# Performance work log

Measured on AMD Instinct MI355X. Metric: run time of the kernel, lower is better.

The kernel has to match this reference:

```python
import jax, jax.numpy as jnp
import numpy as np

N = 100000   # nodes
E = 1600000  # edges
F = 128      # input node features
H = 128      # hidden channels
G = 512      # graphs in batch
EPS = 1e-5   # BatchNorm eps


def setup_inputs() -> dict:
    key = jax.random.key(0)
    ks = jax.random.split(key, 24)
    x = jax.random.normal(ks[0], (N, F), jnp.float32)
    edge_index = jax.random.randint(ks[1], (2, E), 0, N)
    batch = jnp.sort(jax.random.randint(ks[2], (N,), 0, G))

    def lin_w(k, i, o):
        return jax.random.normal(k, (i, o), jnp.float32) / np.sqrt(i)

    inp = {
        "x": x, "edge_index": edge_index, "batch": batch,
        "W1": lin_w(ks[3], F, H), "b1": jnp.zeros((H,), jnp.float32),
        "g1": jnp.ones((H,), jnp.float32), "be1": jnp.zeros((H,), jnp.float32),
        "m1": 0.1 * jax.random.normal(ks[4], (H,), jnp.float32),
        "v1": jax.random.uniform(ks[5], (H,), jnp.float32) + 0.5,
        "W2": lin_w(ks[6], H, H), "b2": jnp.zeros((H,), jnp.float32),
        "g2": jnp.ones((H,), jnp.float32), "be2": jnp.zeros((H,), jnp.float32),
        "m2": 0.1 * jax.random.normal(ks[7], (H,), jnp.float32),
        "v2": jax.random.uniform(ks[8], (H,), jnp.float32) + 0.5,
        "W3": lin_w(ks[9], H, H), "b3": jnp.zeros((H,), jnp.float32),
        "g3": jnp.ones((H,), jnp.float32), "be3": jnp.zeros((H,), jnp.float32),
        "m3": 0.1 * jax.random.normal(ks[10], (H,), jnp.float32),
        "v3": jax.random.uniform(ks[11], (H,), jnp.float32) + 0.5,
        "Wl": lin_w(ks[12], H, 1), "bl": jnp.zeros((1,), jnp.float32),
    }
    return inp


def _gcn_norm(edge_index):
    # add self-loops, then symmetric normalization deg^-1/2 A_hat deg^-1/2
    loops = jnp.arange(N)
    src = jnp.concatenate([edge_index[0], loops])
    dst = jnp.concatenate([edge_index[1], loops])
    deg = jax.ops.segment_sum(jnp.ones_like(src, jnp.float32), dst, num_segments=N)
    dinv = jax.lax.rsqrt(jnp.maximum(deg, 1.0))
    norm = dinv[src] * dinv[dst]  # [E+N]
    return src, dst, norm


def _gcn_conv(x, W, b, src, dst, norm):
    h = x @ W                                    # [N,H] dense GEMM first (PyG order)
    msg = h[src] * norm[:, None]                 # gather + scale, [E+N,H]
    agg = jax.ops.segment_sum(msg, dst, num_segments=N)  # scatter-add
    return agg + b


def _bn_relu(x, g, be, m, v):
    # inference BatchNorm1d (running stats) + ReLU
    return jax.nn.relu((x - m) * jax.lax.rsqrt(v + EPS) * g + be)


def reference(x, edge_index, batch,
              W1, b1, g1, be1, m1, v1,
              W2, b2, g2, be2, m2, v2,
              W3, b3, g3, be3, m3, v3,
              Wl, bl):
    src, dst, norm = _gcn_norm(edge_index)
    h = _bn_relu(_gcn_conv(x, W1, b1, src, dst, norm), g1, be1, m1, v1)
    h = _bn_relu(_gcn_conv(h, W2, b2, src, dst, norm), g2, be2, m2, v2)
    h = _bn_relu(_gcn_conv(h, W3, b3, src, dst, norm), g3, be3, m3, v3)
    # global mean pool over graphs
    sums = jax.ops.segment_sum(h, batch, num_segments=G)           # [G,H]
    cnt = jax.ops.segment_sum(jnp.ones((N,), jnp.float32), batch, num_segments=G)
    pooled = sums / jnp.maximum(cnt, 1.0)[:, None]
    # dropout is identity at inference; final linear
    return pooled @ Wl + bl  # [G,1]
```

## Files before the change

### kernel.cpp

```cpp
#include <hip/hip_runtime.h>
#include <hip/hip_bf16.h>

#define NN 100000
#define NE 1600000
#define HD 128
#define NG 512
#define BN_EPS 1e-5f

typedef __attribute__((ext_vector_type(8))) short short8;
typedef __attribute__((ext_vector_type(4))) float floatx4;

__device__ __forceinline__ ushort f2bf(float f) {
    union { float f; uint u; } v; v.f = f;
    uint r = (v.u + 0x7FFF + ((v.u >> 16) & 1)) >> 16;
    return (ushort)r;
}
__device__ __forceinline__ float bflo(uint u) { union { uint u; float f; } v; v.u = u << 16; return v.f; }
__device__ __forceinline__ float bfhi(uint u) { union { uint u; float f; } v; v.u = u & 0xFFFF0000u; return v.f; }

__global__ void k_zero_i(int* p, int n) {
    int i = blockIdx.x * 256 + threadIdx.x;
    if (i < n) p[i] = 0;
}

__global__ void k_hist_rank(const int* __restrict__ dst, int* __restrict__ indeg,
                            int* __restrict__ rank) {
    int e = blockIdx.x * 256 + threadIdx.x;
    if (e < NE) rank[e] = atomicAdd(&indeg[dst[e]], 1);
}

__global__ void k_dinv(const int* __restrict__ indeg, float* __restrict__ dinv) {
    int i = blockIdx.x * 256 + threadIdx.x;
    if (i < NN) dinv[i] = rsqrtf((float)(indeg[i] + 1));
}

__global__ void k_scan1(const int* __restrict__ indeg, int* __restrict__ rs, int* __restrict__ aux) {
    __shared__ int s[256];
    int t = threadIdx.x;
    int base = blockIdx.x * 1024 + t * 4;
    int v0 = 0, v1 = 0, v2 = 0, v3 = 0;
    if (base + 0 < NN) v0 = indeg[base + 0];
    if (base + 1 < NN) v1 = indeg[base + 1];
    if (base + 2 < NN) v2 = indeg[base + 2];
    if (base + 3 < NN) v3 = indeg[base + 3];
    int tsum = v0 + v1 + v2 + v3;
    s[t] = tsum;
    __syncthreads();
    for (int o = 1; o < 256; o <<= 1) {
        int x = 0;
        if (t >= o) x = s[t - o];
        __syncthreads();
        s[t] += x;
        __syncthreads();
    }
    int excl = s[t] - tsum;
    if (base + 0 < NN) rs[base + 0] = excl;
    if (base + 1 < NN) rs[base + 1] = excl + v0;
    if (base + 2 < NN) rs[base + 2] = excl + v0 + v1;
    if (base + 3 < NN) rs[base + 3] = excl + v0 + v1 + v2;
    if (t == 255) aux[blockIdx.x] = s[255];
}

__global__ void k_scan2(int* __restrict__ aux, int nblk) {
    __shared__ int s[128];
    int t = threadIdx.x;
    int v = (t < nblk) ? aux[t] : 0;
    s[t] = v;
    __syncthreads();
    for (int o = 1; o < 128; o <<= 1) {
        int x = 0;
        if (t >= o) x = s[t - o];
        __syncthreads();
        s[t] += x;
        __syncthreads();
    }
    if (t < nblk) aux[t] = s[t] - v;
}

__global__ void k_scan3(int* __restrict__ rs, const int* __restrict__ aux) {
    int i = blockIdx.x * 256 + threadIdx.x;
    if (i < NN) rs[i] += aux[i >> 10];
    if (i == 0) rs[NN] = NE;
}

__global__ void k_fill(const int* __restrict__ src, const int* __restrict__ dst,
                       const int* __restrict__ rank, const int* __restrict__ rs,
                       int* __restrict__ csr) {
    int e = blockIdx.x * 256 + threadIdx.x;
    if (e >= NE) return;
    csr[rs[dst[e]] + rank[e]] = src[e];
}

__global__ void k_bn_prep(const float* __restrict__ b, const float* __restrict__ g,
                          const float* __restrict__ be, const float* __restrict__ m,
                          const float* __restrict__ v, float* scale, float* shift) {
    int f = threadIdx.x;
    if (f < HD) {
        float sc = g[f] * rsqrtf(v[f] + BN_EPS);
        scale[f] = sc;
        shift[f] = (b[f] - m[f]) * sc + be[f];
    }
}

__global__ void k_gstart(const int* __restrict__ batch, int* __restrict__ gstart) {
    int g = blockIdx.x * 256 + threadIdx.x;
    if (g > NG) return;
    if (g == NG) { gstart[NG] = NN; return; }
    int lo = 0, hi = NN;
    while (lo < hi) {
        int mid = (lo + hi) >> 1;
        if (batch[mid] < g) lo = mid + 1; else hi = mid;
    }
    gstart[g] = lo;
}

__global__ void k_cast(const float* __restrict__ x, ushort* __restrict__ xb) {
    long i = (long)(blockIdx.x * 256 + threadIdx.x) * 4;
    if (i >= (long)NN * 128) return;
    float4 v = *(const float4*)(x + i);
    uint2 o;
    o.x = (uint)f2bf(v.x) | ((uint)f2bf(v.y) << 16);
    o.y = (uint)f2bf(v.z) | ((uint)f2bf(v.w) << 16);
    *(uint2*)(xb + i) = o;
}

#define WT_STRIDE 136
__launch_bounds__(256)
__global__ void k_gemm_mfma(const ushort* __restrict__ xb, const float* __restrict__ W,
                            const float* __restrict__ dinv, ushort* __restrict__ hs) {
    __shared__ ushort sWt[128 * WT_STRIDE];
    const int tid = threadIdx.x;
    for (int i = tid; i < 128 * 128; i += 256) {
        int k = i >> 7, n = i & 127;
        sWt[n * WT_STRIDE + k] = f2bf(W[i]);
    }
    __syncthreads();

    const int wave = tid >> 6, lane = tid & 63;
    const int m = lane & 15, kg = lane >> 4;
    const long row0 = (long)blockIdx.x * 64 + wave * 16;

    long arow = row0 + m;
    long arc = arow < NN ? arow : (NN - 1);
    short8 a[4];
#pragma unroll
    for (int s = 0; s < 4; ++s)
        a[s] = *(const short8*)(xb + arc * 128 + s * 32 + kg * 8);

    floatx4 acc[8];
#pragma unroll
    for (int ct = 0; ct < 8; ++ct) acc[ct] = (floatx4){0.f, 0.f, 0.f, 0.f};

#pragma unroll
    for (int s = 0; s < 4; ++s) {
#pragma unroll
        for (int ct = 0; ct < 8; ++ct) {
            short8 b = *(const short8*)&sWt[(ct * 16 + m) * WT_STRIDE + s * 32 + kg * 8];
            acc[ct] = __builtin_amdgcn_mfma_f32_16x16x32_bf16(a[s], b, acc[ct], 0, 0, 0);
        }
    }

#pragma unroll
    for (int r = 0; r < 4; ++r) {
        long orow = row0 + kg * 4 + r;
        if (orow < NN) {
            float dd = dinv[orow];
#pragma unroll
            for (int ct = 0; ct < 8; ++ct)
                hs[orow * 128 + ct * 16 + m] = f2bf(acc[ct][r] * dd);
        }
    }
}

__global__ void k_gather_bf(const ushort* __restrict__ hs, const int* __restrict__ rs,
                            const int* __restrict__ csr, const float* __restrict__ dinv,
                            const float* __restrict__ scale, const float* __restrict__ shift,
                            ushort* __restrict__ xout) {
    int t = blockIdx.x * 256 + threadIdx.x;
    int d = t >> 4;
    if (d >= NN) return;
    int lane = t & 15;
    int c0 = lane * 8;
    int e0 = rs[d], e1 = rs[d + 1];

    uint4 sv = *(const uint4*)(hs + (long)d * 128 + c0);
    float a0 = bflo(sv.x), a1 = bfhi(sv.x), a2 = bflo(sv.y), a3 = bfhi(sv.y);
    float a4 = bflo(sv.z), a5 = bfhi(sv.z), a6 = bflo(sv.w), a7 = bfhi(sv.w);

    int j = e0;
    for (; j + 1 < e1; j += 2) {
        int s0 = csr[j], s1 = csr[j + 1];
        uint4 v0 = *(const uint4*)(hs + (long)s0 * 128 + c0);
        uint4 v1 = *(const uint4*)(hs + (long)s1 * 128 + c0);
        a0 += bflo(v0.x) + bflo(v1.x); a1 += bfhi(v0.x) + bfhi(v1.x);
        a2 += bflo(v0.y) + bflo(v1.y); a3 += bfhi(v0.y) + bfhi(v1.y);
        a4 += bflo(v0.z) + bflo(v1.z); a5 += bfhi(v0.z) + bfhi(v1.z);
        a6 += bflo(v0.w) + bflo(v1.w); a7 += bfhi(v0.w) + bfhi(v1.w);
    }
    if (j < e1) {
        int s0 = csr[j];
        uint4 v0 = *(const uint4*)(hs + (long)s0 * 128 + c0);
        a0 += bflo(v0.x); a1 += bfhi(v0.x);
        a2 += bflo(v0.y); a3 += bfhi(v0.y);
        a4 += bflo(v0.z); a5 += bfhi(v0.z);
        a6 += bflo(v0.w); a7 += bfhi(v0.w);
    }

    float dd = dinv[d];
    float4 sca = *(const float4*)(scale + c0);
    float4 scb = *(const float4*)(scale + c0 + 4);
    float4 sha = *(const float4*)(shift + c0);
    float4 shb = *(const float4*)(shift + c0 + 4);
    float r0 = fmaxf(dd * a0 * sca.x + sha.x, 0.f);
    float r1 = fmaxf(dd * a1 * sca.y + sha.y, 0.f);
    float r2 = fmaxf(dd * a2 * sca.z + sha.z, 0.f);
    float r3 = fmaxf(dd * a3 * sca.w + sha.w, 0.f);
    float r4 = fmaxf(dd * a4 * scb.x + shb.x, 0.f);
    float r5 = fmaxf(dd * a5 * scb.y + shb.y, 0.f);
    float r6 = fmaxf(dd * a6 * scb.z + shb.z, 0.f);
    float r7 = fmaxf(dd * a7 * scb.w + shb.w, 0.f);
    uint4 o;
    o.x = (uint)f2bf(r0) | ((uint)f2bf(r1) << 16);
    o.y = (uint)f2bf(r2) | ((uint)f2bf(r3) << 16);
    o.z = (uint)f2bf(r4) | ((uint)f2bf(r5) << 16);
    o.w = (uint)f2bf(r6) | ((uint)f2bf(r7) << 16);
    *(uint4*)(xout + (long)d * 128 + c0) = o;
}

__global__ void k_pool_final2(const ushort* __restrict__ x, const int* __restrict__ gstart,
                              const float* __restrict__ Wl, const float* __restrict__ bl,
                              float* __restrict__ out) {
    __shared__ float red[256];
    int g = blockIdx.x;
    int tid = threadIdx.x;
    int f = tid & 127;
    int half = tid >> 7;
    int i0 = gstart[g], i1 = gstart[g + 1];

    float acc = 0.f;
    for (int i = i0 + half; i < i1; i += 2) {
        union { uint u; float f; } v; v.u = (uint)x[(long)i * 128 + f] << 16;
        acc += v.f;
    }
    red[tid] = acc;
    __syncthreads();
    if (tid < 128) red[tid] = (red[tid] + red[tid + 128]) * Wl[tid];
    __syncthreads();
    for (int o = 64; o > 0; o >>= 1) {
        if (tid < o) red[tid] += red[tid + o];
        __syncthreads();
    }
    if (tid == 0) out[g] = red[0] / fmaxf((float)(i1 - i0), 1.f) + bl[0];
}

extern "C" void kernel_launch(void* const* d_in, const int* in_sizes, int n_in,
                              void* d_out, int out_size, void* d_ws, size_t ws_size,
                              hipStream_t stream) {
    const float* x   = (const float*)d_in[0];
    const int*   ei  = (const int*)d_in[1];
    const int*   bat = (const int*)d_in[2];
    const float* W1  = (const float*)d_in[3];
    const float* b1  = (const float*)d_in[4];
    const float* g1  = (const float*)d_in[5];
    const float* be1 = (const float*)d_in[6];
    const float* m1  = (const float*)d_in[7];
    const float* v1  = (const float*)d_in[8];
    const float* W2  = (const float*)d_in[9];
    const float* b2  = (const float*)d_in[10];
    const float* g2  = (const float*)d_in[11];
    const float* be2 = (const float*)d_in[12];
    const float* m2  = (const float*)d_in[13];
    const float* v2  = (const float*)d_in[14];
    const float* W3  = (const float*)d_in[15];
    const float* b3  = (const float*)d_in[16];
    const float* g3  = (const float*)d_in[17];
    const float* be3 = (const float*)d_in[18];
    const float* m3  = (const float*)d_in[19];
    const float* v3  = (const float*)d_in[20];
    const float* Wl  = (const float*)d_in[21];
    const float* bl  = (const float*)d_in[22];
    float* out = (float*)d_out;

    const int* srcp = ei;
    const int* dstp = ei + NE;

    char* ws = (char*)d_ws;
    size_t off = 0;
    auto alloc = [&](size_t bytes) { char* p = ws + off; off += (bytes + 255) & ~255ULL; return p; };
    float*  dinv   = (float*) alloc(NN * 4);
    int*    indeg  = (int*)   alloc(NN * 4);
    int*    rs     = (int*)   alloc((NN + 1) * 4);
    int*    aux    = (int*)   alloc(128 * 4);
    int*    csr    = (int*)   alloc(NE * 4);
    int*    rank   = (int*)   alloc(NE * 4);
    float*  scale1 = (float*) alloc(HD * 4);
    float*  shift1 = (float*) alloc(HD * 4);
    float*  scale2 = (float*) alloc(HD * 4);
    float*  shift2 = (float*) alloc(HD * 4);
    float*  scale3 = (float*) alloc(HD * 4);
    float*  shift3 = (float*) alloc(HD * 4);
    int*    gstart = (int*)   alloc((NG + 1) * 4);
    ushort* xb     = (ushort*)alloc((size_t)NN * HD * 2);
    ushort* hs     = (ushort*)alloc((size_t)NN * HD * 2);
    ushort* xbuf   = (ushort*)alloc((size_t)NN * HD * 2);

    const int nblk_scan = (NN + 1023) / 1024;
    const int grid_n    = (NN + 255) / 256;
    const int grid_e    = (NE + 255) / 256;
    const int gemm_grid = (NN + 63) / 64;
    const int gath_grid = (NN * 16 + 255) / 256;
    const int cast_grid = (NN * 128 / 4 + 255) / 256;

    k_zero_i<<<grid_n, 256, 0, stream>>>(indeg, NN);
    k_hist_rank<<<grid_e, 256, 0, stream>>>(dstp, indeg, rank);
    k_dinv<<<grid_n, 256, 0, stream>>>(indeg, dinv);
    k_scan1<<<nblk_scan, 256, 0, stream>>>(indeg, rs, aux);
    k_scan2<<<1, 128, 0, stream>>>(aux, nblk_scan);
    k_scan3<<<grid_n, 256, 0, stream>>>(rs, aux);
    k_fill<<<grid_e, 256, 0, stream>>>(srcp, dstp, rank, rs, csr);

    k_bn_prep<<<1, 128, 0, stream>>>(b1, g1, be1, m1, v1, scale1, shift1);
    k_bn_prep<<<1, 128, 0, stream>>>(b2, g2, be2, m2, v2, scale2, shift2);
    k_bn_prep<<<1, 128, 0, stream>>>(b3, g3, be3, m3, v3, scale3, shift3);
    k_gstart<<<3, 256, 0, stream>>>(bat, gstart);
    k_cast<<<cast_grid, 256, 0, stream>>>(x, xb);

    k_gemm_mfma<<<gemm_grid, 256, 0, stream>>>(xb, W1, dinv, hs);
    k_gather_bf<<<gath_grid, 256, 0, stream>>>(hs, rs, csr, dinv, scale1, shift1, xbuf);
    k_gemm_mfma<<<gemm_grid, 256, 0, stream>>>(xbuf, W2, dinv, hs);
    k_gather_bf<<<gath_grid, 256, 0, stream>>>(hs, rs, csr, dinv, scale2, shift2, xbuf);
    k_gemm_mfma<<<gemm_grid, 256, 0, stream>>>(xbuf, W3, dinv, hs);
    k_gather_bf<<<gath_grid, 256, 0, stream>>>(hs, rs, csr, dinv, scale3, shift3, xbuf);

    k_pool_final2<<<NG, 256, 0, stream>>>(xbuf, gstart, Wl, bl, out);
}
```

Before: 524.8 us.

## Fuse input cast into GEMM, pretranspose weights, stage epilogue, unroll gather

Removes the separate fp32-to-bf16 cast pass by converting x inside the first GEMM's A-load. Weights are transposed and converted once per layer into global buffers instead of being rebuilt in shared memory by every GEMM block, so B fragments now come from global/L2. The GEMM epilogue is staged through shared memory so rows are written with coalesced 16-byte stores. The gather loop is unrolled to four neighbours for more memory-level parallelism. Reading B from global instead of LDS may add L2 traffic.

```diff
diff --git a/kernel.cpp b/kernel.cpp
--- a/kernel.cpp
+++ b/kernel.cpp
@@ -114,38 +114,47 @@
     gstart[g] = lo;
 }
 
-__global__ void k_cast(const float* __restrict__ x, ushort* __restrict__ xb) {
-    long i = (long)(blockIdx.x * 256 + threadIdx.x) * 4;
-    if (i >= (long)NN * 128) return;
-    float4 v = *(const float4*)(x + i);
-    uint2 o;
-    o.x = (uint)f2bf(v.x) | ((uint)f2bf(v.y) << 16);
-    o.y = (uint)f2bf(v.z) | ((uint)f2bf(v.w) << 16);
-    *(uint2*)(xb + i) = o;
-}
-
-#define WT_STRIDE 136
+__global__ void k_prep_w(const float* __restrict__ W, ushort* __restrict__ Wt) {
+    int i = blockIdx.x * 256 + threadIdx.x;
+    if (i < 128 * 128) {
+        int k = i >> 7, n = i & 127;
+        Wt[n * 128 + k] = f2bf(W[i]);
+    }
+}
+
+template <bool F32>
 __launch_bounds__(256)
-__global__ void k_gemm_mfma(const ushort* __restrict__ xb, const float* __restrict__ W,
-                            const float* __restrict__ dinv, ushort* __restrict__ hs) {
-    __shared__ ushort sWt[128 * WT_STRIDE];
+__global__ void k_gemm(const void* __restrict__ xin, const ushort* __restrict__ Wt,
+                       const float* __restrict__ dinv, ushort* __restrict__ hs) {
+    __shared__ ushort sEp[64 * 128];
     const int tid = threadIdx.x;
-    for (int i = tid; i < 128 * 128; i += 256) {
-        int k = i >> 7, n = i & 127;
-        sWt[n * WT_STRIDE + k] = f2bf(W[i]);
-    }
-    __syncthreads();
-
     const int wave = tid >> 6, lane = tid & 63;
     const int m = lane & 15, kg = lane >> 4;
-    const long row0 = (long)blockIdx.x * 64 + wave * 16;
+    const long rowB = (long)blockIdx.x * 64;
+    const long row0 = rowB + wave * 16;
 
     long arow = row0 + m;
     long arc = arow < NN ? arow : (NN - 1);
     short8 a[4];
-#pragma unroll
-    for (int s = 0; s < 4; ++s)
-        a[s] = *(const short8*)(xb + arc * 128 + s * 32 + kg * 8);
+    if (F32) {
+        const float* xf = (const float*)xin + arc * 128;
+#pragma unroll
+        for (int s = 0; s < 4; ++s) {
+            float4 f0 = *(const float4*)(xf + s * 32 + kg * 8);
+            float4 f1 = *(const float4*)(xf + s * 32 + kg * 8 + 4);
+            short8 t;
+            t[0] = (short)f2bf(f0.x); t[1] = (short)f2bf(f0.y);
+            t[2] = (short)f2bf(f0.z); t[3] = (short)f2bf(f0.w);
+            t[4] = (short)f2bf(f1.x); t[5] = (short)f2bf(f1.y);
+            t[6] = (short)f2bf(f1.z); t[7] = (short)f2bf(f1.w);
+            a[s] = t;
+        }
+    } else {
+        const ushort* xb = (const ushort*)xin + arc * 128;
+#pragma unroll
+        for (int s = 0; s < 4; ++s)
+            a[s] = *(const short8*)(xb + s * 32 + kg * 8);
+    }
 
     floatx4 acc[8];
 #pragma unroll
@@ -155,7 +164,7 @@
     for (int s = 0; s < 4; ++s) {
 #pragma unroll
         for (int ct = 0; ct < 8; ++ct) {
-            short8 b = *(const short8*)&sWt[(ct * 16 + m) * WT_STRIDE + s * 32 + kg * 8];
+            short8 b = *(const short8*)(Wt + (ct * 16 + m) * 128 + s * 32 + kg * 8);
             acc[ct] = __builtin_amdgcn_mfma_f32_16x16x32_bf16(a[s], b, acc[ct], 0, 0, 0);
         }
     }
@@ -163,12 +172,22 @@
 #pragma unroll
     for (int r = 0; r < 4; ++r) {
         long orow = row0 + kg * 4 + r;
-        if (orow < NN) {
-            float dd = dinv[orow];
-#pragma unroll
-            for (int ct = 0; ct < 8; ++ct)
-                hs[orow * 128 + ct * 16 + m] = f2bf(acc[ct][r] * dd);
-        }
+        long orc = orow < NN ? orow : (NN - 1);
+        float dd = dinv[orc];
+#pragma unroll
+        for (int ct = 0; ct < 8; ++ct)
+            sEp[(wave * 16 + kg * 4 + r) * 128 + ct * 16 + m] = f2bf(acc[ct][r] * dd);
+    }
+    __syncthreads();
+
+#pragma unroll
+    for (int it = 0; it < 4; ++it) {
+        int idx = it * 256 + tid;
+        int row = idx >> 4;
+        int col = (idx & 15) * 8;
+        long grow = rowB + row;
+        if (grow < NN)
+            *(uint4*)(hs + grow * 128 + col) = *(const uint4*)&sEp[row * 128 + col];
     }
 }
 
@@ -188,16 +207,22 @@
     float a4 = bflo(sv.z), a5 = bfhi(sv.z), a6 = bflo(sv.w), a7 = bfhi(sv.w);
 
     int j = e0;
-    for (; j + 1 < e1; j += 2) {
-        int s0 = csr[j], s1 = csr[j + 1];
+    for (; j + 3 < e1; j += 4) {
+        int s0 = csr[j], s1 = csr[j + 1], s2 = csr[j + 2], s3 = csr[j + 3];
         uint4 v0 = *(const uint4*)(hs + (long)s0 * 128 + c0);
         uint4 v1 = *(const uint4*)(hs + (long)s1 * 128 + c0);
-        a0 += bflo(v0.x) + bflo(v1.x); a1 += bfhi(v0.x) + bfhi(v1.x);
-        a2 += bflo(v0.y) + bflo(v1.y); a3 += bfhi(v0.y) + bfhi(v1.y);
-        a4 += bflo(v0.z) + bflo(v1.z); a5 += bfhi(v0.z) + bfhi(v1.z);
-        a6 += bflo(v0.w) + bflo(v1.w); a7 += bfhi(v0.w) + bfhi(v1.w);
-    }
-    if (j < e1) {
+        uint4 v2 = *(const uint4*)(hs + (long)s2 * 128 + c0);
+        uint4 v3 = *(const uint4*)(hs + (long)s3 * 128 + c0);
+        a0 += (bflo(v0.x) + bflo(v1.x)) + (bflo(v2.x) + bflo(v3.x));
+        a1 += (bfhi(v0.x) + bfhi(v1.x)) + (bfhi(v2.x) + bfhi(v3.x));
+        a2 += (bflo(v0.y) + bflo(v1.y)) + (bflo(v2.y) + bflo(v3.y));
+        a3 += (bfhi(v0.y) + bfhi(v1.y)) + (bfhi(v2.y) + bfhi(v3.y));
+        a4 += (bflo(v0.z) + bflo(v1.z)) + (bflo(v2.z) + bflo(v3.z));
+        a5 += (bfhi(v0.z) + bfhi(v1.z)) + (bfhi(v2.z) + bfhi(v3.z));
+        a6 += (bflo(v0.w) + bflo(v1.w)) + (bflo(v2.w) + bflo(v3.w));
+        a7 += (bfhi(v0.w) + bfhi(v1.w)) + (bfhi(v2.w) + bfhi(v3.w));
+    }
+    for (; j < e1; ++j) {
         int s0 = csr[j];
         uint4 v0 = *(const uint4*)(hs + (long)s0 * 128 + c0);
         a0 += bflo(v0.x); a1 += bfhi(v0.x);
@@ -300,7 +325,9 @@
     float*  scale3 = (float*) alloc(HD * 4);
     float*  shift3 = (float*) alloc(HD * 4);
     int*    gstart = (int*)   alloc((NG + 1) * 4);
-    ushort* xb     = (ushort*)alloc((size_t)NN * HD * 2);
+    ushort* Wt1    = (ushort*)alloc(128 * 128 * 2);
+    ushort* Wt2    = (ushort*)alloc(128 * 128 * 2);
+    ushort* Wt3    = (ushort*)alloc(128 * 128 * 2);
     ushort* hs     = (ushort*)alloc((size_t)NN * HD * 2);
     ushort* xbuf   = (ushort*)alloc((size_t)NN * HD * 2);
 
@@ -309,7 +336,7 @@
     const int grid_e    = (NE + 255) / 256;
     const int gemm_grid = (NN + 63) / 64;
     const int gath_grid = (NN * 16 + 255) / 256;
-    const int cast_grid = (NN * 128 / 4 + 255) / 256;
+    const int prep_grid = (128 * 128 + 255) / 256;
 
     k_zero_i<<<grid_n, 256, 0, stream>>>(indeg, NN);
     k_hist_rank<<<grid_e, 256, 0, stream>>>(dstp, indeg, rank);
@@ -323,13 +350,15 @@
     k_bn_prep<<<1, 128, 0, stream>>>(b2, g2, be2, m2, v2, scale2, shift2);
     k_bn_prep<<<1, 128, 0, stream>>>(b3, g3, be3, m3, v3, scale3, shift3);
     k_gstart<<<3, 256, 0, stream>>>(bat, gstart);
-    k_cast<<<cast_grid, 256, 0, stream>>>(x, xb);
-
-    k_gemm_mfma<<<gemm_grid, 256, 0, stream>>>(xb, W1, dinv, hs);
+    k_prep_w<<<prep_grid, 256, 0, stream>>>(W1, Wt1);
+    k_prep_w<<<prep_grid, 256, 0, stream>>>(W2, Wt2);
+    k_prep_w<<<prep_grid, 256, 0, stream>>>(W3, Wt3);
+
+    k_gemm<true><<<gemm_grid, 256, 0, stream>>>(x, Wt1, dinv, hs);
     k_gather_bf<<<gath_grid, 256, 0, stream>>>(hs, rs, csr, dinv, scale1, shift1, xbuf);
-    k_gemm_mfma<<<gemm_grid, 256, 0, stream>>>(xbuf, W2, dinv, hs);
+    k_gemm<false><<<gemm_grid, 256, 0, stream>>>(xbuf, Wt2, dinv, hs);
     k_gather_bf<<<gath_grid, 256, 0, stream>>>(hs, rs, csr, dinv, scale2, shift2, xbuf);
-    k_gemm_mfma<<<gemm_grid, 256, 0, stream>>>(xbuf, W3, dinv, hs);
+    k_gemm<false><<<gemm_grid, 256, 0, stream>>>(xbuf, Wt3, dinv, hs);
     k_gather_bf<<<gath_grid, 256, 0, stream>>>(hs, rs, csr, dinv, scale3, shift3, xbuf);
 
     k_pool_final2<<<NG, 256, 0, stream>>>(xbuf, gstart, Wl, bl, out);
```

Result: slower. 560.2 us (+6.7%).
